# Optimization experiments

Hardware: AMD Instinct MI355X
Metric: run time of the kernel (lower is better)

Reference implementation:

```python
import jax, jax.numpy as jnp
import numpy as np

N_SRC1, N_DST1, E1 = 500000, 100000, 1500000
N_DST2, E2 = 20000, 200000
IN_F, H_F, N_CLS = 128, 256, 47


def setup_inputs() -> dict:
    key = jax.random.key(0)
    ks = jax.random.split(key, 12)
    x = jax.random.normal(ks[0], (N_SRC1, IN_F), dtype=jnp.float32)
    W_self1 = jax.random.normal(ks[1], (IN_F, H_F), dtype=jnp.float32) * 0.05
    W_neigh1 = jax.random.normal(ks[2], (IN_F, H_F), dtype=jnp.float32) * 0.05
    b1 = jnp.zeros((H_F,), dtype=jnp.float32)
    W_self2 = jax.random.normal(ks[3], (H_F, N_CLS), dtype=jnp.float32) * 0.05
    W_neigh2 = jax.random.normal(ks[4], (H_F, N_CLS), dtype=jnp.float32) * 0.05
    b2 = jnp.zeros((N_CLS,), dtype=jnp.float32)
    src1 = jax.random.randint(ks[5], (E1,), 0, N_SRC1, dtype=jnp.int64 if jax.config.jax_enable_x64 else jnp.int32)
    dst1 = jax.random.randint(ks[6], (E1,), 0, N_DST1, dtype=src1.dtype)
    src2 = jax.random.randint(ks[7], (E2,), 0, N_DST1, dtype=src1.dtype)
    dst2 = jax.random.randint(ks[8], (E2,), 0, N_DST2, dtype=src1.dtype)
    return {"x": x, "W_self1": W_self1, "W_neigh1": W_neigh1, "b1": b1,
            "W_self2": W_self2, "W_neigh2": W_neigh2, "b2": b2,
            "src1": src1, "dst1": dst1, "src2": src2, "dst2": dst2,
            "n_dst1": N_DST1, "n_dst2": N_DST2}


def _sage_mean(h_src, h_dst, src, dst, n_dst, W_self, W_neigh, b):
    # gather neighbor (src) features along edges, segment-mean into dst nodes
    agg = jax.ops.segment_sum(h_src[src], dst, num_segments=n_dst)  # [n_dst, d]
    deg = jax.ops.segment_sum(jnp.ones_like(dst, dtype=h_src.dtype), dst, num_segments=n_dst)
    h_neigh = agg / jnp.maximum(deg, 1.0)[:, None]
    return h_dst @ W_self + h_neigh @ W_neigh + b


def reference(x, W_self1, W_neigh1, b1, W_self2, W_neigh2, b2,
              src1, dst1, src2, dst2, n_dst1, n_dst2):
    h_dst = x[:n_dst1]
    h = _sage_mean(x, h_dst, src1, dst1, n_dst1, W_self1, W_neigh1, b1)
    h = jax.nn.relu(h)
    h_dst2 = h[:n_dst2]
    out = _sage_mean(h, h_dst2, src2, dst2, n_dst2, W_self2, W_neigh2, b2)
    return out
```

## Files before the change

kernel.cpp:

```cpp
#include <hip/hip_runtime.h>

#define N_SRC1 500000
#define N_DST1 100000
#define E1     1500000
#define N_DST2 20000
#define E2     200000
#define IN_F   128
#define H_F    256
#define N_CLS  47
#define NTOT   120000
#define NB_SCAN 118
#define HIST_B 2930

#define OFF_CNT1  0
#define OFF_CNT2  100000
#define OFF_RP1   120000
#define OFF_RP2   220000
#define OFF_FILL1 240000
#define OFF_FILL2 340000
#define OFF_PART  360000
#define OFF_WT1   360256
#define OFF_WT2   393024
#define OFF_CSR1  417600
#define OFF_CSR2  1917600
#define OFF_AGG1  2117600
#define OFF_H     14917600
#define ZERO_INTS 120000

typedef __attribute__((ext_vector_type(8))) short short8;
typedef __attribute__((ext_vector_type(4))) float floatx4;

static __device__ inline unsigned short f2bf(float f) {
  union { float f; unsigned u; } v; v.f = f;
  unsigned r = v.u + 0x7FFF + ((v.u >> 16) & 1);
  return (unsigned short)(r >> 16);
}
static __device__ inline float bf2f(unsigned short u) {
  union { unsigned u; float f; } v; v.u = ((unsigned)u) << 16;
  return v.f;
}
static __device__ inline void f4acc(float4& a, const float4 b) {
  a.x += b.x; a.y += b.y; a.z += b.z; a.w += b.w;
}

__global__ __launch_bounds__(512) void init_kernel(
    const int* __restrict__ dst1, const int* __restrict__ dst2,
    int* __restrict__ cnt1, int* __restrict__ cnt2,
    const float* __restrict__ Ws1, const float* __restrict__ Wn1,
    unsigned short* __restrict__ Wt,
    const float* __restrict__ Ws2, const float* __restrict__ Wn2,
    unsigned short* __restrict__ Wt2) {
  int bb = blockIdx.x;
  if (bb < HIST_B) {
    int i = bb * 512 + threadIdx.x;
    if (i < E1) atomicAdd(&cnt1[dst1[i]], 1);
    if (i < E2) atomicAdd(&cnt2[dst2[i]], 1);
  } else if (bb < HIST_B + 128) {
    int q = bb - HIST_B;
    int n = q * 2 + (threadIdx.x >> 8);
    int k = threadIdx.x & 255;
    float v = (k < IN_F) ? Ws1[k * H_F + n] : Wn1[(k - IN_F) * H_F + n];
    Wt[n * 256 + k] = f2bf(v);
  } else {
    int n = bb - HIST_B - 128;
    int k = threadIdx.x;
    float v = 0.f;
    if (n < N_CLS) v = (k < H_F) ? Ws2[k * N_CLS + n] : Wn2[(k - H_F) * N_CLS + n];
    Wt2[n * 512 + k] = f2bf(v);
  }
}

__global__ __launch_bounds__(1024) void scanA_kernel(
    const int* __restrict__ cnt, int* __restrict__ part) {
  __shared__ int wsum[16];
  int i = blockIdx.x * 1024 + threadIdx.x;
  int v = (i < NTOT) ? cnt[i] : 0;
  int lane = threadIdx.x & 63, wid = threadIdx.x >> 6;
#pragma unroll
  for (int off = 1; off < 64; off <<= 1) v += __shfl_xor(v, off, 64);
  if (lane == 0) wsum[wid] = v;
  __syncthreads();
  if (threadIdx.x == 0) {
    int s = 0;
#pragma unroll
    for (int w = 0; w < 16; ++w) s += wsum[w];
    part[blockIdx.x] = s;
  }
}

__global__ __launch_bounds__(64) void scanB_kernel(int* __restrict__ part) {
  int lane = threadIdx.x;
  int i1 = 64 + lane;
  int v0 = (lane < NB_SCAN) ? part[lane] : 0;
  int v1 = (i1 < NB_SCAN) ? part[i1] : 0;
  int s0 = v0;
#pragma unroll
  for (int off = 1; off < 64; off <<= 1) {
    int t = __shfl_up(s0, off, 64);
    if (lane >= off) s0 += t;
  }
  int total0 = __shfl(s0, 63, 64);
  int s1 = v1;
#pragma unroll
  for (int off = 1; off < 64; off <<= 1) {
    int t = __shfl_up(s1, off, 64);
    if (lane >= off) s1 += t;
  }
  if (lane < NB_SCAN) part[lane] = s0 - v0;
  if (i1 < NB_SCAN)   part[i1]   = total0 + s1 - v1;
}

__global__ __launch_bounds__(1024) void scanC_kernel(
    const int* __restrict__ cnt, const int* __restrict__ part,
    int* __restrict__ rp1, int* __restrict__ rp2,
    int* __restrict__ fill1, int* __restrict__ fill2) {
  __shared__ int wsum[16];
  int i = blockIdx.x * 1024 + threadIdx.x;
  int v = (i < NTOT) ? cnt[i] : 0;
  int lane = threadIdx.x & 63, wid = threadIdx.x >> 6;
  int s = v;
#pragma unroll
  for (int off = 1; off < 64; off <<= 1) {
    int t = __shfl_up(s, off, 64);
    if (lane >= off) s += t;
  }
  if (lane == 63) wsum[wid] = s;
  __syncthreads();
  if (threadIdx.x == 0) {
    int run = part[blockIdx.x];
#pragma unroll
    for (int w = 0; w < 16; ++w) { int t = wsum[w]; wsum[w] = run; run += t; }
  }
  __syncthreads();
  int excl = s - v + wsum[wid];
  if (i < N_DST1)      { rp1[i] = excl;          fill1[i] = excl; }
  else if (i < NTOT)   { rp2[i - N_DST1] = excl - E1; fill2[i - N_DST1] = excl - E1; }
}

__global__ __launch_bounds__(256) void scatter_kernel(
    const int* __restrict__ src1, const int* __restrict__ dst1,
    const int* __restrict__ src2, const int* __restrict__ dst2,
    int* __restrict__ fill1, int* __restrict__ fill2,
    int* __restrict__ csr1, int* __restrict__ csr2) {
  int i = blockIdx.x * 256 + threadIdx.x;
  if (i < E1) {
    int p = atomicAdd(&fill1[dst1[i]], 1);
    csr1[p] = src1[i];
  }
  if (i < E2) {
    int p = atomicAdd(&fill2[dst2[i]], 1);
    csr2[p] = src2[i];
  }
}

__global__ __launch_bounds__(256) void reduce1_kernel(
    const float* __restrict__ x, const int* __restrict__ csr,
    const int* __restrict__ rowptr, const int* __restrict__ cnt,
    unsigned short* __restrict__ aggb) {
  int w = (blockIdx.x * 256 + threadIdx.x) >> 6;
  if (w >= N_DST1) return;
  int lane = threadIdx.x & 63;
  int slot = lane >> 5;
  int f4   = lane & 31;
  const int* __restrict__ cp = csr + rowptr[w];
  int n = cnt[w];
  float4 a0 = make_float4(0.f,0.f,0.f,0.f), a1 = a0, a2 = a0, a3 = a0;
  int j = slot;
  for (; j + 6 < n; j += 8) {
    int s0 = cp[j];
    int s1 = cp[j + 2];
    int s2 = cp[j + 4];
    int s3 = cp[j + 6];
    float4 v0 = ((const float4*)(x + (size_t)s0 * IN_F))[f4];
    float4 v1 = ((const float4*)(x + (size_t)s1 * IN_F))[f4];
    float4 v2 = ((const float4*)(x + (size_t)s2 * IN_F))[f4];
    float4 v3 = ((const float4*)(x + (size_t)s3 * IN_F))[f4];
    f4acc(a0, v0); f4acc(a1, v1); f4acc(a2, v2); f4acc(a3, v3);
  }
  for (; j < n; j += 2) {
    int s = cp[j];
    float4 v = ((const float4*)(x + (size_t)s * IN_F))[f4];
    f4acc(a0, v);
  }
  f4acc(a0, a1); f4acc(a2, a3); f4acc(a0, a2);
  a0.x += __shfl(a0.x, lane ^ 32, 64);
  a0.y += __shfl(a0.y, lane ^ 32, 64);
  a0.z += __shfl(a0.z, lane ^ 32, 64);
  a0.w += __shfl(a0.w, lane ^ 32, 64);
  if (lane < 32) {
    float inv = 1.f / fmaxf((float)n, 1.f);
    ushort4 o;
    o.x = f2bf(a0.x * inv); o.y = f2bf(a0.y * inv);
    o.z = f2bf(a0.z * inv); o.w = f2bf(a0.w * inv);
    ((ushort4*)(aggb + (size_t)w * IN_F))[f4] = o;
  }
}

#define ASTR 264
#define WSTR 40
__global__ __launch_bounds__(256) void layer1_mfma_kernel(
    const float* __restrict__ x, const unsigned short* __restrict__ aggb,
    const unsigned short* __restrict__ Wt,
    const float* __restrict__ b, unsigned short* __restrict__ h) {
  __shared__ __align__(16) unsigned short As[64 * ASTR];
  __shared__ __align__(16) unsigned short Wl[256 * WSTR];
  int t    = threadIdx.x;
  int row0 = blockIdx.x * 64;
#pragma unroll
  for (int i = 0; i < 8; ++i) {
    int g = t + i * 256;
    int r = g >> 5, seg = g & 31, k0 = seg * 8;
    int grow = row0 + r;
    uint4 p;
    if (grow < N_DST1) {
      if (k0 < IN_F) {
        float4 v0 = ((const float4*)(x + (size_t)grow * IN_F + k0))[0];
        float4 v1 = ((const float4*)(x + (size_t)grow * IN_F + k0))[1];
        p.x = (unsigned)f2bf(v0.x) | ((unsigned)f2bf(v0.y) << 16);
        p.y = (unsigned)f2bf(v0.z) | ((unsigned)f2bf(v0.w) << 16);
        p.z = (unsigned)f2bf(v1.x) | ((unsigned)f2bf(v1.y) << 16);
        p.w = (unsigned)f2bf(v1.z) | ((unsigned)f2bf(v1.w) << 16);
      } else {
        p = *((const uint4*)(aggb + (size_t)grow * IN_F + (k0 - IN_F)));
      }
    } else {
      p.x = p.y = p.z = p.w = 0u;
    }
    *((uint4*)(As + r * ASTR + seg * 8)) = p;
  }

  floatx4 acc[4][4] = {};
  int wid = t >> 6, lane = t & 63;
  int quad = lane >> 4, l15 = lane & 15;

  for (int kc = 0; kc < 8; ++kc) {
    int k0 = kc * 32;
    __syncthreads();
#pragma unroll
    for (int rep = 0; rep < 4; ++rep) {
      int flat = t + rep * 256;
      int n = flat >> 2, part = flat & 3;
      *((uint4*)(Wl + n * WSTR + part * 8)) =
          *((const uint4*)(Wt + n * 256 + k0 + part * 8));
    }
    __syncthreads();
    short8 af[4], bfr[4];
#pragma unroll
    for (int mi = 0; mi < 4; ++mi)
      af[mi] = *((const short8*)(As + (mi * 16 + l15) * ASTR + k0 + quad * 8));
#pragma unroll
    for (int ni = 0; ni < 4; ++ni)
      bfr[ni] = *((const short8*)(Wl + (wid * 64 + ni * 16 + l15) * WSTR + quad * 8));
#pragma unroll
    for (int mi = 0; mi < 4; ++mi)
#pragma unroll
      for (int ni = 0; ni < 4; ++ni)
        acc[mi][ni] = __builtin_amdgcn_mfma_f32_16x16x32_bf16(
            af[mi], bfr[ni], acc[mi][ni], 0, 0, 0);
  }

  float bv[4];
#pragma unroll
  for (int ni = 0; ni < 4; ++ni) bv[ni] = b[wid * 64 + ni * 16 + l15];
#pragma unroll
  for (int mi = 0; mi < 4; ++mi) {
    int rbase = row0 + mi * 16 + quad * 4;
#pragma unroll
    for (int r = 0; r < 4; ++r) {
      int row = rbase + r;
      if (row < N_DST1) {
#pragma unroll
        for (int ni = 0; ni < 4; ++ni)
          h[(size_t)row * H_F + wid * 64 + ni * 16 + l15] =
              f2bf(fmaxf(acc[mi][ni][r] + bv[ni], 0.f));
      }
    }
  }
}

__global__ __launch_bounds__(256) void reduce2_kernel(
    const unsigned short* __restrict__ h, const int* __restrict__ csr,
    const int* __restrict__ rowptr, const int* __restrict__ cnt,
    unsigned short* __restrict__ agg2b) {
  int w = (blockIdx.x * 256 + threadIdx.x) >> 6;
  if (w >= N_DST2) return;
  int lane = threadIdx.x & 63;
  const int* __restrict__ cp = csr + rowptr[w];
  int n = cnt[w];
  float4 a0 = make_float4(0.f,0.f,0.f,0.f), a1 = a0, a2 = a0, a3 = a0;
  int j = 0;
  for (; j + 3 < n; j += 4) {
    int s0 = cp[j], s1 = cp[j + 1], s2 = cp[j + 2], s3 = cp[j + 3];
    ushort4 v0 = *((const ushort4*)(h + (size_t)s0 * H_F + lane * 4));
    ushort4 v1 = *((const ushort4*)(h + (size_t)s1 * H_F + lane * 4));
    ushort4 v2 = *((const ushort4*)(h + (size_t)s2 * H_F + lane * 4));
    ushort4 v3 = *((const ushort4*)(h + (size_t)s3 * H_F + lane * 4));
    a0.x += bf2f(v0.x); a0.y += bf2f(v0.y); a0.z += bf2f(v0.z); a0.w += bf2f(v0.w);
    a1.x += bf2f(v1.x); a1.y += bf2f(v1.y); a1.z += bf2f(v1.z); a1.w += bf2f(v1.w);
    a2.x += bf2f(v2.x); a2.y += bf2f(v2.y); a2.z += bf2f(v2.z); a2.w += bf2f(v2.w);
    a3.x += bf2f(v3.x); a3.y += bf2f(v3.y); a3.z += bf2f(v3.z); a3.w += bf2f(v3.w);
  }
  for (; j < n; ++j) {
    int s = cp[j];
    ushort4 v = *((const ushort4*)(h + (size_t)s * H_F + lane * 4));
    a0.x += bf2f(v.x); a0.y += bf2f(v.y); a0.z += bf2f(v.z); a0.w += bf2f(v.w);
  }
  f4acc(a0, a1); f4acc(a2, a3); f4acc(a0, a2);
  float inv = 1.f / fmaxf((float)n, 1.f);
  ushort4 o;
  o.x = f2bf(a0.x * inv); o.y = f2bf(a0.y * inv);
  o.z = f2bf(a0.z * inv); o.w = f2bf(a0.w * inv);
  ((ushort4*)(agg2b + (size_t)w * H_F))[lane] = o;
}

__global__ __launch_bounds__(256) void layer2_mfma_kernel(
    const unsigned short* __restrict__ h,
    const unsigned short* __restrict__ agg2b,
    const unsigned short* __restrict__ Wt2,
    const float* __restrict__ b, float* __restrict__ out) {
  int t = threadIdx.x;
  int wid = t >> 6, lane = t & 63;
  int quad = lane >> 4, l15 = lane & 15;
  int base = blockIdx.x * 64 + wid * 16;
  if (base >= N_DST2) return;
  int arow = base + l15;
  floatx4 acc[3] = {};

  for (int kc = 0; kc < 8; ++kc) {
    short8 af = *((const short8*)(h + (size_t)arow * H_F + kc * 32 + quad * 8));
#pragma unroll
    for (int nt = 0; nt < 3; ++nt) {
      short8 bf = *((const short8*)(Wt2 + (nt * 16 + l15) * 512 + kc * 32 + quad * 8));
      acc[nt] = __builtin_amdgcn_mfma_f32_16x16x32_bf16(af, bf, acc[nt], 0, 0, 0);
    }
  }
  for (int kc = 0; kc < 8; ++kc) {
    short8 af = *((const short8*)(agg2b + (size_t)arow * H_F + kc * 32 + quad * 8));
#pragma unroll
    for (int nt = 0; nt < 3; ++nt) {
      short8 bf = *((const short8*)(Wt2 + (nt * 16 + l15) * 512 + 256 + kc * 32 + quad * 8));
      acc[nt] = __builtin_amdgcn_mfma_f32_16x16x32_bf16(af, bf, acc[nt], 0, 0, 0);
    }
  }
#pragma unroll
  for (int nt = 0; nt < 3; ++nt) {
    int col = nt * 16 + l15;
    if (col < N_CLS) {
      float bv = b[col];
#pragma unroll
      for (int r = 0; r < 4; ++r) {
        int orow = base + quad * 4 + r;
        out[(size_t)orow * N_CLS + col] = acc[nt][r] + bv;
      }
    }
  }
}

extern "C" void kernel_launch(void* const* d_in, const int* in_sizes, int n_in,
                              void* d_out, int out_size, void* d_ws, size_t ws_size,
                              hipStream_t stream) {
  const float* x   = (const float*)d_in[0];
  const float* Ws1 = (const float*)d_in[1];
  const float* Wn1 = (const float*)d_in[2];
  const float* b1  = (const float*)d_in[3];
  const float* Ws2 = (const float*)d_in[4];
  const float* Wn2 = (const float*)d_in[5];
  const float* b2  = (const float*)d_in[6];
  const int* src1  = (const int*)d_in[7];
  const int* dst1  = (const int*)d_in[8];
  const int* src2  = (const int*)d_in[9];
  const int* dst2  = (const int*)d_in[10];

  int*   wsI  = (int*)d_ws;
  int*   cnt1  = wsI + OFF_CNT1;
  int*   cnt2  = wsI + OFF_CNT2;
  int*   rp1   = wsI + OFF_RP1;
  int*   rp2   = wsI + OFF_RP2;
  int*   fill1 = wsI + OFF_FILL1;
  int*   fill2 = wsI + OFF_FILL2;
  int*   part  = wsI + OFF_PART;
  unsigned short* Wt    = (unsigned short*)(wsI + OFF_WT1);
  unsigned short* Wt2   = (unsigned short*)(wsI + OFF_WT2);
  int*   csr1  = wsI + OFF_CSR1;
  int*   csr2  = wsI + OFF_CSR2;
  unsigned short* aggb  = (unsigned short*)(wsI + OFF_AGG1);
  unsigned short* agg2b = (unsigned short*)(wsI + OFF_AGG1);
  unsigned short* h = (unsigned short*)(wsI + OFF_H);
  float* out   = (float*)d_out;

  hipMemsetAsync(wsI, 0, (size_t)ZERO_INTS * sizeof(int), stream);

  init_kernel<<<HIST_B + 128 + 48, 512, 0, stream>>>(
      dst1, dst2, cnt1, cnt2, Ws1, Wn1, Wt, Ws2, Wn2, Wt2);
  scanA_kernel<<<NB_SCAN, 1024, 0, stream>>>(cnt1, part);
  scanB_kernel<<<1, 64, 0, stream>>>(part);
  scanC_kernel<<<NB_SCAN, 1024, 0, stream>>>(cnt1, part, rp1, rp2, fill1, fill2);
  {
    int blocks = (E1 + 255) / 256;
    scatter_kernel<<<blocks, 256, 0, stream>>>(src1, dst1, src2, dst2,
                                               fill1, fill2, csr1, csr2);
  }
  {
    int blocks = (N_DST1 * 64 + 255) / 256;
    reduce1_kernel<<<blocks, 256, 0, stream>>>(x, csr1, rp1, cnt1, aggb);
  }
  {
    int blocks = (N_DST1 + 63) / 64;
    layer1_mfma_kernel<<<blocks, 256, 0, stream>>>(x, aggb, Wt, b1, h);
  }
  {
    int blocks = (N_DST2 * 64 + 255) / 256;
    reduce2_kernel<<<blocks, 256, 0, stream>>>(h, csr2, rp2, cnt2, agg2b);
  }
  {
    int blocks = (N_DST2 + 63) / 64;
    layer2_mfma_kernel<<<blocks, 256, 0, stream>>>(h, agg2b, Wt2, b2, out);
  }
}
```

Before: 717.1 us.

## Fuse three-pass scan into one block and fold layer-2 gather into GEMM

Replaces the three-kernel prefix scan over the degree counts with a single 1024-thread block in which each thread serially sums and writes 118 counts, removing two launches. The layer-2 neighbour mean is computed inside the layer-2 MFMA kernel and staged in padded shared memory, so the separate reduce kernel and its global round trip are gone. In exchange the scan runs on one CU with strided, uncoalesced per-thread loops. The fused layer-2 kernel runs 313 blocks, each wave serially gathering 16 rows, which lowers parallelism for the gather phase.

New measurement: 999.0 us. 1.39x slower.

```diff
diff --git a/kernel.cpp b/kernel.cpp
--- a/kernel.cpp
+++ b/kernel.cpp
@@ -9,7 +9,6 @@
 #define H_F    256
 #define N_CLS  47
 #define NTOT   120000
-#define NB_SCAN 118
 #define HIST_B 2930
 
 #define OFF_CNT1  0
@@ -18,7 +17,6 @@
 #define OFF_RP2   220000
 #define OFF_FILL1 240000
 #define OFF_FILL2 340000
-#define OFF_PART  360000
 #define OFF_WT1   360256
 #define OFF_WT2   393024
 #define OFF_CSR1  417600
@@ -70,71 +68,38 @@
   }
 }
 
-__global__ __launch_bounds__(1024) void scanA_kernel(
-    const int* __restrict__ cnt, int* __restrict__ part) {
-  __shared__ int wsum[16];
-  int i = blockIdx.x * 1024 + threadIdx.x;
-  int v = (i < NTOT) ? cnt[i] : 0;
-  int lane = threadIdx.x & 63, wid = threadIdx.x >> 6;
-#pragma unroll
-  for (int off = 1; off < 64; off <<= 1) v += __shfl_xor(v, off, 64);
-  if (lane == 0) wsum[wid] = v;
-  __syncthreads();
-  if (threadIdx.x == 0) {
-    int s = 0;
-#pragma unroll
-    for (int w = 0; w < 16; ++w) s += wsum[w];
-    part[blockIdx.x] = s;
-  }
-}
-
-__global__ __launch_bounds__(64) void scanB_kernel(int* __restrict__ part) {
-  int lane = threadIdx.x;
-  int i1 = 64 + lane;
-  int v0 = (lane < NB_SCAN) ? part[lane] : 0;
-  int v1 = (i1 < NB_SCAN) ? part[i1] : 0;
-  int s0 = v0;
-#pragma unroll
-  for (int off = 1; off < 64; off <<= 1) {
-    int t = __shfl_up(s0, off, 64);
-    if (lane >= off) s0 += t;
-  }
-  int total0 = __shfl(s0, 63, 64);
-  int s1 = v1;
-#pragma unroll
-  for (int off = 1; off < 64; off <<= 1) {
-    int t = __shfl_up(s1, off, 64);
-    if (lane >= off) s1 += t;
-  }
-  if (lane < NB_SCAN) part[lane] = s0 - v0;
-  if (i1 < NB_SCAN)   part[i1]   = total0 + s1 - v1;
-}
-
-__global__ __launch_bounds__(1024) void scanC_kernel(
-    const int* __restrict__ cnt, const int* __restrict__ part,
+__global__ __launch_bounds__(1024) void scan_fused_kernel(
+    const int* __restrict__ cnt,
     int* __restrict__ rp1, int* __restrict__ rp2,
     int* __restrict__ fill1, int* __restrict__ fill2) {
-  __shared__ int wsum[16];
-  int i = blockIdx.x * 1024 + threadIdx.x;
-  int v = (i < NTOT) ? cnt[i] : 0;
-  int lane = threadIdx.x & 63, wid = threadIdx.x >> 6;
-  int s = v;
+  __shared__ int wtot[16];
+  int t = threadIdx.x;
+  int beg = t * 118;
+  int end = beg + 118; if (end > NTOT) end = NTOT;
+  int s = 0;
+  for (int i = beg; i < end; ++i) s += cnt[i];
+  int lane = t & 63, wid = t >> 6;
+  int ps = s;
 #pragma unroll
   for (int off = 1; off < 64; off <<= 1) {
-    int t = __shfl_up(s, off, 64);
-    if (lane >= off) s += t;
-  }
-  if (lane == 63) wsum[wid] = s;
+    int u = __shfl_up(ps, off, 64);
+    if (lane >= off) ps += u;
+  }
+  if (lane == 63) wtot[wid] = ps;
   __syncthreads();
-  if (threadIdx.x == 0) {
-    int run = part[blockIdx.x];
-#pragma unroll
-    for (int w = 0; w < 16; ++w) { int t = wsum[w]; wsum[w] = run; run += t; }
+  if (t == 0) {
+    int run = 0;
+#pragma unroll
+    for (int w = 0; w < 16; ++w) { int tmp = wtot[w]; wtot[w] = run; run += tmp; }
   }
   __syncthreads();
-  int excl = s - v + wsum[wid];
-  if (i < N_DST1)      { rp1[i] = excl;          fill1[i] = excl; }
-  else if (i < NTOT)   { rp2[i - N_DST1] = excl - E1; fill2[i - N_DST1] = excl - E1; }
+  int run = ps - s + wtot[wid];
+  for (int i = beg; i < end; ++i) {
+    int v = cnt[i];
+    if (i < N_DST1) { rp1[i] = run;            fill1[i] = run; }
+    else            { rp2[i - N_DST1] = run - E1; fill2[i - N_DST1] = run - E1; }
+    run += v;
+  }
 }
 
 __global__ __launch_bounds__(256) void scatter_kernel(
@@ -278,54 +243,57 @@
   }
 }
 
-__global__ __launch_bounds__(256) void reduce2_kernel(
-    const unsigned short* __restrict__ h, const int* __restrict__ csr,
-    const int* __restrict__ rowptr, const int* __restrict__ cnt,
-    unsigned short* __restrict__ agg2b) {
-  int w = (blockIdx.x * 256 + threadIdx.x) >> 6;
-  if (w >= N_DST2) return;
-  int lane = threadIdx.x & 63;
-  const int* __restrict__ cp = csr + rowptr[w];
-  int n = cnt[w];
-  float4 a0 = make_float4(0.f,0.f,0.f,0.f), a1 = a0, a2 = a0, a3 = a0;
-  int j = 0;
-  for (; j + 3 < n; j += 4) {
-    int s0 = cp[j], s1 = cp[j + 1], s2 = cp[j + 2], s3 = cp[j + 3];
-    ushort4 v0 = *((const ushort4*)(h + (size_t)s0 * H_F + lane * 4));
-    ushort4 v1 = *((const ushort4*)(h + (size_t)s1 * H_F + lane * 4));
-    ushort4 v2 = *((const ushort4*)(h + (size_t)s2 * H_F + lane * 4));
-    ushort4 v3 = *((const ushort4*)(h + (size_t)s3 * H_F + lane * 4));
-    a0.x += bf2f(v0.x); a0.y += bf2f(v0.y); a0.z += bf2f(v0.z); a0.w += bf2f(v0.w);
-    a1.x += bf2f(v1.x); a1.y += bf2f(v1.y); a1.z += bf2f(v1.z); a1.w += bf2f(v1.w);
-    a2.x += bf2f(v2.x); a2.y += bf2f(v2.y); a2.z += bf2f(v2.z); a2.w += bf2f(v2.w);
-    a3.x += bf2f(v3.x); a3.y += bf2f(v3.y); a3.z += bf2f(v3.z); a3.w += bf2f(v3.w);
-  }
-  for (; j < n; ++j) {
-    int s = cp[j];
-    ushort4 v = *((const ushort4*)(h + (size_t)s * H_F + lane * 4));
-    a0.x += bf2f(v.x); a0.y += bf2f(v.y); a0.z += bf2f(v.z); a0.w += bf2f(v.w);
-  }
-  f4acc(a0, a1); f4acc(a2, a3); f4acc(a0, a2);
-  float inv = 1.f / fmaxf((float)n, 1.f);
-  ushort4 o;
-  o.x = f2bf(a0.x * inv); o.y = f2bf(a0.y * inv);
-  o.z = f2bf(a0.z * inv); o.w = f2bf(a0.w * inv);
-  ((ushort4*)(agg2b + (size_t)w * H_F))[lane] = o;
-}
-
-__global__ __launch_bounds__(256) void layer2_mfma_kernel(
+#define L2ASTR 264
+__global__ __launch_bounds__(256) void layer2_fused_kernel(
     const unsigned short* __restrict__ h,
-    const unsigned short* __restrict__ agg2b,
+    const int* __restrict__ csr, const int* __restrict__ rowptr,
+    const int* __restrict__ cnt,
     const unsigned short* __restrict__ Wt2,
     const float* __restrict__ b, float* __restrict__ out) {
+  __shared__ __align__(16) unsigned short An[64 * L2ASTR];
   int t = threadIdx.x;
   int wid = t >> 6, lane = t & 63;
   int quad = lane >> 4, l15 = lane & 15;
-  int base = blockIdx.x * 64 + wid * 16;
+  int blk = blockIdx.x * 64;
+
+  for (int rr = 0; rr < 16; ++rr) {
+    int r = wid * 16 + rr;
+    int d = blk + r;
+    if (d < N_DST2) {
+      const int* __restrict__ cp = csr + rowptr[d];
+      int n = cnt[d];
+      float4 a0 = make_float4(0.f,0.f,0.f,0.f), a1 = a0, a2 = a0, a3 = a0;
+      int j = 0;
+      for (; j + 3 < n; j += 4) {
+        int s0 = cp[j], s1 = cp[j + 1], s2 = cp[j + 2], s3 = cp[j + 3];
+        ushort4 v0 = *((const ushort4*)(h + (size_t)s0 * H_F + lane * 4));
+        ushort4 v1 = *((const ushort4*)(h + (size_t)s1 * H_F + lane * 4));
+        ushort4 v2 = *((const ushort4*)(h + (size_t)s2 * H_F + lane * 4));
+        ushort4 v3 = *((const ushort4*)(h + (size_t)s3 * H_F + lane * 4));
+        a0.x += bf2f(v0.x); a0.y += bf2f(v0.y); a0.z += bf2f(v0.z); a0.w += bf2f(v0.w);
+        a1.x += bf2f(v1.x); a1.y += bf2f(v1.y); a1.z += bf2f(v1.z); a1.w += bf2f(v1.w);
+        a2.x += bf2f(v2.x); a2.y += bf2f(v2.y); a2.z += bf2f(v2.z); a2.w += bf2f(v2.w);
+        a3.x += bf2f(v3.x); a3.y += bf2f(v3.y); a3.z += bf2f(v3.z); a3.w += bf2f(v3.w);
+      }
+      for (; j < n; ++j) {
+        int s = cp[j];
+        ushort4 v = *((const ushort4*)(h + (size_t)s * H_F + lane * 4));
+        a0.x += bf2f(v.x); a0.y += bf2f(v.y); a0.z += bf2f(v.z); a0.w += bf2f(v.w);
+      }
+      f4acc(a0, a1); f4acc(a2, a3); f4acc(a0, a2);
+      float inv = 1.f / fmaxf((float)n, 1.f);
+      ushort4 o;
+      o.x = f2bf(a0.x * inv); o.y = f2bf(a0.y * inv);
+      o.z = f2bf(a0.z * inv); o.w = f2bf(a0.w * inv);
+      *((ushort4*)(An + r * L2ASTR + lane * 4)) = o;
+    }
+  }
+  __syncthreads();
+
+  int base = blk + wid * 16;
   if (base >= N_DST2) return;
   int arow = base + l15;
   floatx4 acc[3] = {};
-
   for (int kc = 0; kc < 8; ++kc) {
     short8 af = *((const short8*)(h + (size_t)arow * H_F + kc * 32 + quad * 8));
 #pragma unroll
@@ -335,7 +303,7 @@
     }
   }
   for (int kc = 0; kc < 8; ++kc) {
-    short8 af = *((const short8*)(agg2b + (size_t)arow * H_F + kc * 32 + quad * 8));
+    short8 af = *((const short8*)(An + (wid * 16 + l15) * L2ASTR + kc * 32 + quad * 8));
 #pragma unroll
     for (int nt = 0; nt < 3; ++nt) {
       short8 bf = *((const short8*)(Wt2 + (nt * 16 + l15) * 512 + 256 + kc * 32 + quad * 8));
@@ -378,13 +346,11 @@
   int*   rp2   = wsI + OFF_RP2;
   int*   fill1 = wsI + OFF_FILL1;
   int*   fill2 = wsI + OFF_FILL2;
-  int*   part  = wsI + OFF_PART;
   unsigned short* Wt    = (unsigned short*)(wsI + OFF_WT1);
   unsigned short* Wt2   = (unsigned short*)(wsI + OFF_WT2);
   int*   csr1  = wsI + OFF_CSR1;
   int*   csr2  = wsI + OFF_CSR2;
   unsigned short* aggb  = (unsigned short*)(wsI + OFF_AGG1);
-  unsigned short* agg2b = (unsigned short*)(wsI + OFF_AGG1);
   unsigned short* h = (unsigned short*)(wsI + OFF_H);
   float* out   = (float*)d_out;
 
@@ -392,9 +358,7 @@
 
   init_kernel<<<HIST_B + 128 + 48, 512, 0, stream>>>(
       dst1, dst2, cnt1, cnt2, Ws1, Wn1, Wt, Ws2, Wn2, Wt2);
-  scanA_kernel<<<NB_SCAN, 1024, 0, stream>>>(cnt1, part);
-  scanB_kernel<<<1, 64, 0, stream>>>(part);
-  scanC_kernel<<<NB_SCAN, 1024, 0, stream>>>(cnt1, part, rp1, rp2, fill1, fill2);
+  scan_fused_kernel<<<1, 1024, 0, stream>>>(cnt1, rp1, rp2, fill1, fill2);
   {
     int blocks = (E1 + 255) / 256;
     scatter_kernel<<<blocks, 256, 0, stream>>>(src1, dst1, src2, dst2,
@@ -409,11 +373,7 @@
     layer1_mfma_kernel<<<blocks, 256, 0, stream>>>(x, aggb, Wt, b1, h);
   }
   {
-    int blocks = (N_DST2 * 64 + 255) / 256;
-    reduce2_kernel<<<blocks, 256, 0, stream>>>(h, csr2, rp2, cnt2, agg2b);
-  }
-  {
     int blocks = (N_DST2 + 63) / 64;
-    layer2_mfma_kernel<<<blocks, 256, 0, stream>>>(h, agg2b, Wt2, b2, out);
-  }
-}
+    layer2_fused_kernel<<<blocks, 256, 0, stream>>>(h, csr2, rp2, cnt2, Wt2, b2, out);
+  }
+}
```
